# Optimization experiments

Measured on AMD Instinct MI355X. Metric: run time of the kernel, lower is better.

## Reference

```python
import jax, jax.numpy as jnp
import numpy as np

N_NODES = 245760      # 8192 graphs * 30 atoms
N_GRAPHS = 8192
N_EDGES = 1000000
NODES_PER_GRAPH = 30
F_NODE = 78
F_CELL = 1000
HID = 64


def _lin(key, fan_in, fan_out):
    kw, kb = jax.random.split(key)
    s = 1.0 / np.sqrt(fan_in)
    W = jax.random.uniform(kw, (fan_in, fan_out), minval=-s, maxval=s, dtype=jnp.float32)
    b = jax.random.uniform(kb, (fan_out,), minval=-s, maxval=s, dtype=jnp.float32)
    return W, b


def setup_inputs() -> dict:
    key = jax.random.key(0)
    ks = jax.random.split(key, 14)
    x = jax.random.normal(ks[0], (N_NODES, F_NODE), dtype=jnp.float32)
    # edges constrained within each graph: node = graph_id * 30 + local offset
    offs = jax.random.randint(ks[1], (2, N_EDGES), 0, NODES_PER_GRAPH)
    ge = jax.random.randint(ks[2], (N_EDGES,), 0, N_GRAPHS)
    edge_index = (ge[None, :] * NODES_PER_GRAPH + offs).astype(jnp.int64)
    batch = jnp.repeat(jnp.arange(N_GRAPHS, dtype=jnp.int64), NODES_PER_GRAPH)
    cell_features = jax.random.normal(ks[3], (N_GRAPHS, F_CELL), dtype=jnp.float32)
    W1, b1 = _lin(ks[4], F_NODE, HID)
    W2, b2 = _lin(ks[5], HID, 2 * HID)
    W3, b3 = _lin(ks[6], 2 * HID, 4 * HID)
    Wd, bd = _lin(ks[7], 4 * HID, HID)          # drug_embed_fc
    Wc1, bc1 = _lin(ks[8], F_CELL, 2 * HID)      # cell_fc1
    Wc2, bc2 = _lin(ks[9], 2 * HID, HID)         # cell_fc2
    Wm1, bm1 = _lin(ks[10], 2 * HID, HID)        # combiner_fc1
    Wm2, bm2 = _lin(ks[11], HID, 32)             # combiner_fc2
    Wo, bo = _lin(ks[12], 32, 1)                 # output_fc
    return {"x": x, "edge_index": edge_index, "batch": batch,
            "cell_features": cell_features,
            "W1": W1, "b1": b1, "W2": W2, "b2": b2, "W3": W3, "b3": b3,
            "Wd": Wd, "bd": bd, "Wc1": Wc1, "bc1": bc1, "Wc2": Wc2, "bc2": bc2,
            "Wm1": Wm1, "bm1": bm1, "Wm2": Wm2, "bm2": bm2, "Wo": Wo, "bo": bo}


def _gcn_conv(h, W, b, srcA, dstA, norm, n_nodes):
    # PyG GCNConv: linear transform, then sym-normalized scatter-add (self-loops included in srcA/dstA/norm)
    h = h @ W                                   # [N, out]
    msg = h[srcA] * norm[:, None]               # gather + edge scaling
    out = jnp.zeros((n_nodes, W.shape[1]), h.dtype).at[dstA].add(msg)
    return out + b


def reference(x, edge_index, batch, cell_features,
              W1, b1, W2, b2, W3, b3, Wd, bd,
              Wc1, bc1, Wc2, bc2, Wm1, bm1, Wm2, bm2, Wo, bo):
    n = x.shape[0]
    loops = jnp.arange(n, dtype=edge_index.dtype)
    srcA = jnp.concatenate([edge_index[0], loops])
    dstA = jnp.concatenate([edge_index[1], loops])
    deg = jax.ops.segment_sum(jnp.ones_like(dstA, dtype=x.dtype), dstA, num_segments=n)
    dinv = jax.lax.rsqrt(deg)                   # deg >= 1 due to self-loops
    norm = dinv[srcA] * dinv[dstA]

    h = jax.nn.relu(_gcn_conv(x, W1, b1, srcA, dstA, norm, n))
    h = jax.nn.relu(_gcn_conv(h, W2, b2, srcA, dstA, norm, n))
    h = jax.nn.relu(_gcn_conv(h, W3, b3, srcA, dstA, norm, n))

    # global mean pool over graphs
    sums = jax.ops.segment_sum(h, batch, num_segments=N_GRAPHS)
    cnts = jax.ops.segment_sum(jnp.ones((n,), h.dtype), batch, num_segments=N_GRAPHS)
    drug = (sums / cnts[:, None]) @ Wd + bd     # [B, HID]

    cell = jax.nn.relu(cell_features @ Wc1 + bc1)
    cell = cell @ Wc2 + bc2                      # [B, HID]

    comb = jnp.concatenate([drug, cell], axis=1)
    z = jax.nn.relu(comb @ Wm1 + bm1)
    z = jax.nn.relu(z @ Wm2 + bm2)
    out = z @ Wo + bo
    return out.reshape(-1)
```

## Files before the change

kernel.cpp:

```cpp
#include <hip/hip_runtime.h>

typedef __attribute__((ext_vector_type(8))) short short8;
typedef __attribute__((ext_vector_type(4))) short short4v;
typedef __attribute__((ext_vector_type(4))) float f32x4;
typedef unsigned short u16;

__device__ __forceinline__ u16 f2bf(float f) {
    union { float f; unsigned u; } v; v.f = f;
    unsigned r = v.u + 0x7FFFu + ((v.u >> 16) & 1u);
    return (u16)(r >> 16);
}
__device__ __forceinline__ float bf2f(u16 h) {
    union { unsigned u; float f; } v; v.u = ((unsigned)h) << 16;
    return v.f;
}
__device__ __forceinline__ void split2(float f, u16& h, u16& l) {
    h = f2bf(f);
    l = f2bf(f - bf2f(h));
}
__device__ __forceinline__ short8 ld8(const u16* p) {
    short4v a = *(const short4v*)p;
    short4v b = *(const short4v*)(p + 4);
    short8 r;
    r[0] = a[0]; r[1] = a[1]; r[2] = a[2]; r[3] = a[3];
    r[4] = b[0]; r[5] = b[1]; r[6] = b[2]; r[7] = b[3];
    return r;
}
#define MFMA(A, B, C) __builtin_amdgcn_mfma_f32_16x16x32_bf16(A, B, C, 0, 0, 0)

__global__ __launch_bounds__(256) void k_prep(int4* __restrict__ A32z, int nz4,
        const float* __restrict__ W1, u16* __restrict__ W1h, u16* __restrict__ W1l,
        const float* __restrict__ W2, u16* __restrict__ W2h, u16* __restrict__ W2l,
        const float* __restrict__ W3, u16* __restrict__ W3h, u16* __restrict__ W3l,
        const float* __restrict__ Wc1, u16* __restrict__ Wc1h, u16* __restrict__ Wc1l,
        const float* __restrict__ Wd, u16* __restrict__ WdTh, u16* __restrict__ WdTl,
        const float* __restrict__ Wc2, u16* __restrict__ Wc2Th, u16* __restrict__ Wc2Tl,
        const float* __restrict__ Wm1, u16* __restrict__ Wm1Th, u16* __restrict__ Wm1Tl,
        const float* __restrict__ Wm2, u16* __restrict__ Wm2Th, u16* __restrict__ Wm2Tl) {
    int i = blockIdx.x * 256 + threadIdx.x;
    if (i < nz4) { A32z[i] = make_int4(0, 0, 0, 0); return; }
    i -= nz4;
    const float* W; u16 *th, *tl; int K, F, Kp;
    if (i < 6144)        { W = W1;  th = W1h;  tl = W1l;  K = 78;   F = 64;  Kp = 96; }
    else if (i < 14336)  { i -= 6144;   W = W2;  th = W2h;  tl = W2l;  K = 64;   F = 128; Kp = 64; }
    else if (i < 47104)  { i -= 14336;  W = W3;  th = W3h;  tl = W3l;  K = 128;  F = 256; Kp = 128; }
    else if (i < 178176) { i -= 47104;  W = Wc1; th = Wc1h; tl = Wc1l; K = 1000; F = 128; Kp = 1024; }
    else if (i < 194560) { i -= 178176; W = Wd;  th = WdTh; tl = WdTl; K = 256;  F = 64;  Kp = 256; }
    else if (i < 202752) { i -= 194560; W = Wc2; th = Wc2Th; tl = Wc2Tl; K = 128; F = 64; Kp = 128; }
    else if (i < 210944) { i -= 202752; W = Wm1; th = Wm1Th; tl = Wm1Tl; K = 128; F = 64; Kp = 128; }
    else if (i < 212992) { i -= 210944; W = Wm2; th = Wm2Th; tl = Wm2Tl; K = 64;  F = 32; Kp = 64; }
    else return;
    int f = i / Kp, k = i - f * Kp;
    float v = (k < K) ? W[(size_t)k * F + f] : 0.f;
    u16 h, l; split2(v, h, l);
    th[i] = h; tl[i] = l;
}

__global__ void k_cnt(const int* __restrict__ ei, unsigned* __restrict__ A32, int E) {
    int e = blockIdx.x * 256 + threadIdx.x;
    if (e >= E) return;
    int s = ei[e], d = ei[E + e];
    int g = d / 30;
    int idx = g * 960 + (d - g * 30) * 32 + (s - g * 30);
    atomicAdd(&A32[idx >> 1], 1u << ((idx & 1) * 16));
}

__global__ __launch_bounds__(512, 8) void k_nodecell(
    const float* __restrict__ x, const unsigned* __restrict__ A32,
    const u16* __restrict__ W1h, const u16* __restrict__ W1l,
    const u16* __restrict__ W2h, const u16* __restrict__ W2l,
    const u16* __restrict__ W3h, const u16* __restrict__ W3l,
    const float* __restrict__ b1, const float* __restrict__ b2,
    const float* __restrict__ b3, float* __restrict__ P,
    const float* __restrict__ cf,
    const u16* __restrict__ Wc1h, const u16* __restrict__ Wc1l,
    const float* __restrict__ bc1, float* __restrict__ cell1,
    int CELLB) {
    __shared__ __align__(16) char smem[39936];
    int t = threadIdx.x;
    int wave = t >> 6, lane = t & 63, quad = lane >> 4, l15 = lane & 15;

    if (blockIdx.x < CELLB) {
        u16* Xh = (u16*)(smem + 0);
        u16* Xl = (u16*)(smem + 17920);
        int row0 = blockIdx.x * 64;
        int half = wave >> 2, wq = wave & 3;
        f32x4 acc[2][2] = {{{0.f,0.f,0.f,0.f},{0.f,0.f,0.f,0.f}},
                           {{0.f,0.f,0.f,0.f},{0.f,0.f,0.f,0.f}}};
        for (int ko = 0; ko < 8; ko++) {
#pragma unroll
            for (int ii = 0; ii < 4; ii++) {
                int i = t + ii * 512;
                int r = i >> 5, c4 = i & 31;
                int col = ko * 128 + c4 * 4;
                float4 v = {0.f, 0.f, 0.f, 0.f};
                if (col < 1000) v = *(const float4*)(cf + (size_t)(row0 + r) * 1000 + col);
                float vv[4] = {v.x, v.y, v.z, v.w};
                short4v hs, ls;
#pragma unroll
                for (int j = 0; j < 4; j++) {
                    u16 h, l; split2(vv[j], h, l);
                    hs[j] = (short)h; ls[j] = (short)l;
                }
                *(short4v*)(Xh + r * 140 + c4 * 4) = hs;
                *(short4v*)(Xl + r * 140 + c4 * 4) = ls;
            }
            __syncthreads();
#pragma unroll
            for (int kk = 0; kk < 4; kk++) {
                int klo = kk * 32 + quad * 8;
                short8 ah[2], al[2];
#pragma unroll
                for (int mi = 0; mi < 2; mi++) {
                    ah[mi] = ld8(&Xh[(half * 32 + mi * 16 + l15) * 140 + klo]);
                    al[mi] = ld8(&Xl[(half * 32 + mi * 16 + l15) * 140 + klo]);
                }
#pragma unroll
                for (int ni = 0; ni < 2; ni++) {
                    int col = wq * 32 + ni * 16 + l15;
                    size_t o = (size_t)col * 1024 + ko * 128 + kk * 32 + quad * 8;
                    short8 bh = *(const short8*)(Wc1h + o);
                    short8 bl = *(const short8*)(Wc1l + o);
#pragma unroll
                    for (int mi = 0; mi < 2; mi++) {
                        acc[mi][ni] = MFMA(ah[mi], bh, acc[mi][ni]);
                        acc[mi][ni] = MFMA(al[mi], bh, acc[mi][ni]);
                        acc[mi][ni] = MFMA(ah[mi], bl, acc[mi][ni]);
                    }
                }
            }
            __syncthreads();
        }
#pragma unroll
        for (int ni = 0; ni < 2; ni++) {
            int col = wq * 32 + ni * 16 + l15;
            float bv = bc1[col];
#pragma unroll
            for (int mi = 0; mi < 2; mi++)
#pragma unroll
                for (int rg = 0; rg < 4; rg++) {
                    int row = row0 + half * 32 + mi * 16 + quad * 4 + rg;
                    cell1[(size_t)row * 128 + col] = fmaxf(acc[mi][ni][rg] + bv, 0.f);
                }
        }
        return;
    }

    int g = blockIdx.x - CELLB;
    u16* xh  = (u16*)(smem + 0);
    u16* xl  = (u16*)(smem + 6400);
    u16* h1h = (u16*)(smem + 0);
    u16* h1l = (u16*)(smem + 4352);
    u16* a3h = (u16*)(smem + 0);
    u16* a3l = (u16*)(smem + 8448);
    float* Afp = (float*)(smem + 16896);
    float* dv  = (float*)(smem + 20736);
    u16* t1h = (u16*)(smem + 16896);
    u16* t1l = (u16*)(smem + 21504);
    u16* h2h = (u16*)(smem + 16896);
    u16* h2l = (u16*)(smem + 26112);
    u16* Ah  = (u16*)(smem + 35328);
    u16* Al  = (u16*)(smem + 37632);

    {
        for (int i = t; i < 860; i += 512) {
            uint* arr = (uint*)((i >= 430) ? (char*)xl : (char*)xh);
            int j = (i >= 430) ? i - 430 : i;
            int r, c32;
            if (j < 330) { r = j / 11; c32 = 39 + j % 11; }
            else { r = 30 + (j - 330) / 50; c32 = (j - 330) % 50; }
            arr[r * 50 + c32] = 0;
        }
        const float4* xg = (const float4*)(x + (size_t)g * 2340);
        for (int i = t; i < 585; i += 512) {
            float4 v = xg[i];
            int base = i * 4;
            float vv[4] = {v.x, v.y, v.z, v.w};
#pragma unroll
            for (int j = 0; j < 4; j++) {
                int idx = base + j;
                int r = idx / 78, c = idx - r * 78;
                u16 h, l; split2(vv[j], h, l);
                xh[r * 100 + c] = h; xl[r * 100 + c] = l;
            }
        }
        const unsigned* ac = A32 + (size_t)g * 480;
        for (int i = t; i < 480; i += 512) {
            unsigned w = ac[i];
            Afp[2 * i] = (float)(w & 0xFFFFu);
            Afp[2 * i + 1] = (float)(w >> 16);
        }
        if (t < 32) {
            float s = 1.f;
            if (t < 30) {
                const unsigned* rp = ac + t * 16;
                unsigned acc = 0;
#pragma unroll
                for (int j = 0; j < 16; j++) { unsigned w = rp[j]; acc += (w & 0xFFFFu) + (w >> 16); }
                s += (float)acc;
            }
            dv[t] = (t < 30) ? rsqrtf(s) : 0.f;
        }
    }
    __syncthreads();
    {
#pragma unroll
        for (int ii = 0; ii < 2; ii++) {
            int i = t + ii * 512;
            int r = i >> 5, c = i & 31;
            float a = 0.f;
            if (r < 30 && c < 30)
                a = (Afp[r * 32 + c] + (r == c ? 1.f : 0.f)) * dv[r] * dv[c];
            u16 h, l; split2(a, h, l);
            Ah[r * 36 + c] = h; Al[r * 36 + c] = l;
        }
    }
    __syncthreads();
    {
        int wm = wave >> 2, wn = wave & 3;
        int arow = wm * 16 + l15;
        int col = wn * 16 + l15;
        const u16* wph = W1h + col * 96 + quad * 8;
        const u16* wpl = W1l + col * 96 + quad * 8;
        f32x4 acc = {0.f, 0.f, 0.f, 0.f};
#pragma unroll
        for (int ch = 0; ch < 3; ch++) {
            int kc = ch * 32;
            short8 bh = *(const short8*)(wph + kc);
            short8 bl = *(const short8*)(wpl + kc);
            short8 ah = ld8(&xh[arow * 100 + kc + quad * 8]);
            short8 al = ld8(&xl[arow * 100 + kc + quad * 8]);
            acc = MFMA(ah, bh, acc);
            acc = MFMA(al, bh, acc);
            acc = MFMA(ah, bl, acc);
        }
#pragma unroll
        for (int rg = 0; rg < 4; rg++) {
            int row = wm * 16 + quad * 4 + rg;
            u16 h, l; split2(acc[rg], h, l);
            t1h[col * 36 + row] = h;
            t1l[col * 36 + row] = l;
        }
    }
    __syncthreads();
    {
        int wm = wave >> 2, wn = wave & 3;
        int arow = wm * 16 + l15;
        int col = wn * 16 + l15;
        short8 aAh = ld8(&Ah[arow * 36 + quad * 8]);
        short8 aAl = ld8(&Al[arow * 36 + quad * 8]);
        short8 bh = ld8(&t1h[col * 36 + quad * 8]);
        short8 bl = ld8(&t1l[col * 36 + quad * 8]);
        f32x4 acc = {0.f, 0.f, 0.f, 0.f};
        acc = MFMA(aAh, bh, acc);
        acc = MFMA(aAl, bh, acc);
        acc = MFMA(aAh, bl, acc);
        float bb = b1[col];
#pragma unroll
        for (int rg = 0; rg < 4; rg++) {
            int row = wm * 16 + quad * 4 + rg;
            float v = fmaxf(acc[rg] + bb, 0.f);
            u16 h, l; split2(v, h, l);
            h1h[row * 68 + col] = h;
            h1l[row * 68 + col] = l;
        }
    }
    __syncthreads();
    {
        int col = wave * 16 + l15;
        const u16* wph = W2h + col * 64 + quad * 8;
        const u16* wpl = W2l + col * 64 + quad * 8;
        f32x4 acc[2] = {{0.f,0.f,0.f,0.f},{0.f,0.f,0.f,0.f}};
#pragma unroll
        for (int ch = 0; ch < 2; ch++) {
            int kc = ch * 32;
            short8 bh = *(const short8*)(wph + kc);
            short8 bl = *(const short8*)(wpl + kc);
#pragma unroll
            for (int mi = 0; mi < 2; mi++) {
                short8 ah = ld8(&h1h[(mi * 16 + l15) * 68 + kc + quad * 8]);
                short8 al = ld8(&h1l[(mi * 16 + l15) * 68 + kc + quad * 8]);
                acc[mi] = MFMA(ah, bh, acc[mi]);
                acc[mi] = MFMA(al, bh, acc[mi]);
                acc[mi] = MFMA(ah, bl, acc[mi]);
            }
        }
        float bb = b2[col];
#pragma unroll
        for (int mi = 0; mi < 2; mi++)
#pragma unroll
            for (int rg = 0; rg < 4; rg++) {
                int row = mi * 16 + quad * 4 + rg;
                float v = fmaxf(acc[mi][rg] + bb, 0.f);
                u16 h, l; split2(v, h, l);
                h2h[col * 36 + row] = h;
                h2l[col * 36 + row] = l;
            }
    }
    __syncthreads();
    {
        int col = wave * 16 + l15;
        short8 bh = ld8(&h2h[col * 36 + quad * 8]);
        short8 bl = ld8(&h2l[col * 36 + quad * 8]);
        f32x4 acc[2] = {{0.f,0.f,0.f,0.f},{0.f,0.f,0.f,0.f}};
#pragma unroll
        for (int mi = 0; mi < 2; mi++) {
            short8 aAh = ld8(&Ah[(mi * 16 + l15) * 36 + quad * 8]);
            short8 aAl = ld8(&Al[(mi * 16 + l15) * 36 + quad * 8]);
            acc[mi] = MFMA(aAh, bh, acc[mi]);
            acc[mi] = MFMA(aAl, bh, acc[mi]);
            acc[mi] = MFMA(aAh, bl, acc[mi]);
        }
#pragma unroll
        for (int mi = 0; mi < 2; mi++)
#pragma unroll
            for (int rg = 0; rg < 4; rg++) {
                int row = mi * 16 + quad * 4 + rg;
                u16 h, l; split2(acc[mi][rg], h, l);
                a3h[row * 132 + col] = h;
                a3l[row * 132 + col] = l;
            }
    }
    __syncthreads();
    {
        int colb = wave * 32;
        f32x4 acc[2][2] = {{{0.f,0.f,0.f,0.f},{0.f,0.f,0.f,0.f}},
                           {{0.f,0.f,0.f,0.f},{0.f,0.f,0.f,0.f}}};
        short8 cwh[2], cwl[2], nwh[2], nwl[2];
#pragma unroll
        for (int ni = 0; ni < 2; ni++) {
            size_t o = (size_t)(colb + ni * 16 + l15) * 128 + quad * 8;
            cwh[ni] = *(const short8*)(W3h + o);
            cwl[ni] = *(const short8*)(W3l + o);
        }
#pragma unroll
        for (int ch = 0; ch < 4; ch++) {
            if (ch < 3) {
#pragma unroll
                for (int ni = 0; ni < 2; ni++) {
                    size_t o = (size_t)(colb + ni * 16 + l15) * 128 + (ch + 1) * 32 + quad * 8;
                    nwh[ni] = *(const short8*)(W3h + o);
                    nwl[ni] = *(const short8*)(W3l + o);
                }
            }
            short8 ah[2], al[2];
#pragma unroll
            for (int mi = 0; mi < 2; mi++) {
                ah[mi] = ld8(&a3h[(mi * 16 + l15) * 132 + ch * 32 + quad * 8]);
                al[mi] = ld8(&a3l[(mi * 16 + l15) * 132 + ch * 32 + quad * 8]);
            }
#pragma unroll
            for (int mi = 0; mi < 2; mi++)
#pragma unroll
                for (int ni = 0; ni < 2; ni++) {
                    acc[mi][ni] = MFMA(ah[mi], cwh[ni], acc[mi][ni]);
                    acc[mi][ni] = MFMA(al[mi], cwh[ni], acc[mi][ni]);
                    acc[mi][ni] = MFMA(ah[mi], cwl[ni], acc[mi][ni]);
                }
            if (ch < 3) {
#pragma unroll
                for (int ni = 0; ni < 2; ni++) { cwh[ni] = nwh[ni]; cwl[ni] = nwl[ni]; }
            }
        }
#pragma unroll
        for (int ni = 0; ni < 2; ni++) {
            int col = colb + ni * 16 + l15;
            float bb = b3[col];
            float p = 0.f;
#pragma unroll
            for (int mi = 0; mi < 2; mi++)
#pragma unroll
                for (int rg = 0; rg < 4; rg++) {
                    int row = mi * 16 + quad * 4 + rg;
                    if (row < 30) p += fmaxf(acc[mi][ni][rg] + bb, 0.f);
                }
            p += __shfl_down(p, 32);
            p += __shfl_down(p, 16);
            if (lane < 16)
                P[(size_t)g * 256 + colb + ni * 16 + lane] = p * (1.0f / 30.0f);
        }
    }
}

__global__ __launch_bounds__(256) void k_tail2(const float* __restrict__ pooled,
        const float* __restrict__ cell1,
        const u16* __restrict__ WdTh, const u16* __restrict__ WdTl, const float* __restrict__ bd,
        const u16* __restrict__ Wc2Th, const u16* __restrict__ Wc2Tl, const float* __restrict__ bc2,
        const u16* __restrict__ Wm1Th, const u16* __restrict__ Wm1Tl, const float* __restrict__ bm1,
        const u16* __restrict__ Wm2Th, const u16* __restrict__ Wm2Tl, const float* __restrict__ bm2,
        const float* __restrict__ Wo, const float* __restrict__ bo,
        float* __restrict__ out) {
    __shared__ __align__(16) char smem[50176];
    u16* Xh  = (u16*)(smem);
    u16* Xl  = (u16*)(smem + 25088);
    u16* dzh = (u16*)(smem);
    u16* dzl = (u16*)(smem + 8960);
    u16* z1h = (u16*)(smem + 17920);
    u16* z1l = (u16*)(smem + 22528);
    float* z2f = (float*)(smem + 27136);
    int t = threadIdx.x;
    int row0 = blockIdx.x * 32;
    int wave = t >> 6, lane = t & 63, quad = lane >> 4, l15 = lane & 15;

#pragma unroll
    for (int ii = 0; ii < 12; ii++) {
        int i = t + ii * 256;
        int r = i / 96, c4 = i - r * 96;
        float4 v = (c4 < 64)
            ? ((const float4*)(pooled + (size_t)(row0 + r) * 256))[c4]
            : ((const float4*)(cell1 + (size_t)(row0 + r) * 128))[c4 - 64];
        float vv[4] = {v.x, v.y, v.z, v.w};
        short4v hs, ls;
#pragma unroll
        for (int j = 0; j < 4; j++) {
            u16 h, l; split2(vv[j], h, l);
            hs[j] = (short)h; ls[j] = (short)l;
        }
        *(short4v*)(Xh + r * 392 + c4 * 4) = hs;
        *(short4v*)(Xl + r * 392 + c4 * 4) = ls;
    }
    __syncthreads();

    bool cw = wave >= 2;
    int nbase = (wave & 1) * 32;
    const u16* Bh = cw ? Wc2Th : WdTh;
    const u16* Bl = cw ? Wc2Tl : WdTl;
    const int Kp = cw ? 128 : 256;
    const int nch = cw ? 4 : 8;
    const int acol = cw ? 256 : 0;
    f32x4 acc[2][2] = {{{0.f,0.f,0.f,0.f},{0.f,0.f,0.f,0.f}},
                       {{0.f,0.f,0.f,0.f},{0.f,0.f,0.f,0.f}}};
    for (int ch = 0; ch < nch; ch++) {
        int kc = ch * 32 + quad * 8;
        short8 ah[2], al[2];
#pragma unroll
        for (int mi = 0; mi < 2; mi++) {
            ah[mi] = ld8(&Xh[(mi * 16 + l15) * 392 + acol + kc]);
            al[mi] = ld8(&Xl[(mi * 16 + l15) * 392 + acol + kc]);
        }
#pragma unroll
        for (int ni = 0; ni < 2; ni++) {
            int col = nbase + ni * 16 + l15;
            short8 bh = *(const short8*)(Bh + (size_t)col * Kp + kc);
            short8 bl = *(const short8*)(Bl + (size_t)col * Kp + kc);
#pragma unroll
            for (int mi = 0; mi < 2; mi++) {
                acc[mi][ni] = MFMA(ah[mi], bh, acc[mi][ni]);
                acc[mi][ni] = MFMA(al[mi], bh, acc[mi][ni]);
                acc[mi][ni] = MFMA(ah[mi], bl, acc[mi][ni]);
            }
        }
    }
    __syncthreads();
#pragma unroll
    for (int ni = 0; ni < 2; ni++) {
        int c = nbase + ni * 16 + l15;
        float bb = cw ? bc2[c] : bd[c];
        int col = (cw ? 64 : 0) + c;
#pragma unroll
        for (int mi = 0; mi < 2; mi++)
#pragma unroll
            for (int rg = 0; rg < 4; rg++) {
                int row = mi * 16 + quad * 4 + rg;
                u16 h, l; split2(acc[mi][ni][rg] + bb, h, l);
                dzh[row * 140 + col] = h;
                dzl[row * 140 + col] = l;
            }
    }
    __syncthreads();

    {
        int col = wave * 16 + l15;
        f32x4 a2[2] = {{0.f,0.f,0.f,0.f},{0.f,0.f,0.f,0.f}};
#pragma unroll
        for (int ch = 0; ch < 4; ch++) {
            int kc = ch * 32 + quad * 8;
            short8 bh = *(const short8*)(Wm1Th + (size_t)col * 128 + kc);
            short8 bl = *(const short8*)(Wm1Tl + (size_t)col * 128 + kc);
#pragma unroll
            for (int mi = 0; mi < 2; mi++) {
                short8 ah = ld8(&dzh[(mi * 16 + l15) * 140 + kc]);
                short8 al = ld8(&dzl[(mi * 16 + l15) * 140 + kc]);
                a2[mi] = MFMA(ah, bh, a2[mi]);
                a2[mi] = MFMA(al, bh, a2[mi]);
                a2[mi] = MFMA(ah, bl, a2[mi]);
            }
        }
        float bb = bm1[col];
#pragma unroll
        for (int mi = 0; mi < 2; mi++)
#pragma unroll
            for (int rg = 0; rg < 4; rg++) {
                int row = mi * 16 + quad * 4 + rg;
                u16 h, l; split2(fmaxf(a2[mi][rg] + bb, 0.f), h, l);
                z1h[row * 72 + col] = h;
                z1l[row * 72 + col] = l;
            }
    }
    __syncthreads();

    if (wave < 2) {
        int col = wave * 16 + l15;
        f32x4 a3[2] = {{0.f,0.f,0.f,0.f},{0.f,0.f,0.f,0.f}};
#pragma unroll
        for (int ch = 0; ch < 2; ch++) {
            int kc = ch * 32 + quad * 8;
            short8 bh = *(const short8*)(Wm2Th + (size_t)col * 64 + kc);
            short8 bl = *(const short8*)(Wm2Tl + (size_t)col * 64 + kc);
#pragma unroll
            for (int mi = 0; mi < 2; mi++) {
                short8 ah = ld8(&z1h[(mi * 16 + l15) * 72 + kc]);
                short8 al = ld8(&z1l[(mi * 16 + l15) * 72 + kc]);
                a3[mi] = MFMA(ah, bh, a3[mi]);
                a3[mi] = MFMA(al, bh, a3[mi]);
                a3[mi] = MFMA(ah, bl, a3[mi]);
            }
        }
        float bb = bm2[col];
#pragma unroll
        for (int mi = 0; mi < 2; mi++)
#pragma unroll
            for (int rg = 0; rg < 4; rg++) {
                int row = mi * 16 + quad * 4 + rg;
                z2f[row * 33 + col] = fmaxf(a3[mi][rg] + bb, 0.f);
            }
    }
    __syncthreads();

    if (t < 32) {
        float s = bo[0];
#pragma unroll 8
        for (int k = 0; k < 32; k++) s += z2f[t * 33 + k] * Wo[k];
        out[row0 + t] = s;
    }
}


extern "C" void kernel_launch(void* const* d_in, const int* in_sizes, int n_in,
                              void* d_out, int out_size, void* d_ws, size_t ws_size,
                              hipStream_t stream) {
    const float* x   = (const float*)d_in[0];
    const int*   ei  = (const int*)d_in[1];
    const float* cf  = (const float*)d_in[3];
    const float* W1  = (const float*)d_in[4];
    const float* b1  = (const float*)d_in[5];
    const float* W2  = (const float*)d_in[6];
    const float* b2  = (const float*)d_in[7];
    const float* W3  = (const float*)d_in[8];
    const float* b3  = (const float*)d_in[9];
    const float* Wd  = (const float*)d_in[10];
    const float* bd  = (const float*)d_in[11];
    const float* Wc1 = (const float*)d_in[12];
    const float* bc1 = (const float*)d_in[13];
    const float* Wc2 = (const float*)d_in[14];
    const float* bc2 = (const float*)d_in[15];
    const float* Wm1 = (const float*)d_in[16];
    const float* bm1 = (const float*)d_in[17];
    const float* Wm2 = (const float*)d_in[18];
    const float* bm2 = (const float*)d_in[19];
    const float* Wo  = (const float*)d_in[20];
    const float* bo  = (const float*)d_in[21];
    float* out = (float*)d_out;

    const int E = in_sizes[1] / 2;
    const int B = in_sizes[3] / 1000;

    char* w = (char*)d_ws;
    auto carve = [&](size_t bytes) { void* p = (void*)w; w += (bytes + 255) & ~(size_t)255; return p; };
    unsigned* A32 = (unsigned*)carve((size_t)B * 960 * 2);
    float* pooled = (float*)carve((size_t)B * 256 * 4);
    float* cell1  = (float*)carve((size_t)B * 128 * 4);
    u16* W1th = (u16*)carve(64 * 96 * 2);     u16* W1tl = (u16*)carve(64 * 96 * 2);
    u16* W2th = (u16*)carve(128 * 64 * 2);    u16* W2tl = (u16*)carve(128 * 64 * 2);
    u16* W3th = (u16*)carve(256 * 128 * 2);   u16* W3tl = (u16*)carve(256 * 128 * 2);
    u16* Wc1th = (u16*)carve(128 * 1024 * 2); u16* Wc1tl = (u16*)carve(128 * 1024 * 2);
    u16* WdTh = (u16*)carve(64 * 256 * 2);    u16* WdTl = (u16*)carve(64 * 256 * 2);
    u16* Wc2Th = (u16*)carve(64 * 128 * 2);   u16* Wc2Tl = (u16*)carve(64 * 128 * 2);
    u16* Wm1Th = (u16*)carve(64 * 128 * 2);   u16* Wm1Tl = (u16*)carve(64 * 128 * 2);
    u16* Wm2Th = (u16*)carve(32 * 64 * 2);    u16* Wm2Tl = (u16*)carve(32 * 64 * 2);

    auto g1 = [](int n) { return (n + 255) / 256; };

    const int nz4 = B * 120;
    const int nsplit = 212992;

    k_prep<<<g1(nz4 + nsplit), 256, 0, stream>>>((int4*)A32, nz4,
        W1, W1th, W1tl, W2, W2th, W2tl, W3, W3th, W3tl, Wc1, Wc1th, Wc1tl,
        Wd, WdTh, WdTl, Wc2, Wc2Th, Wc2Tl, Wm1, Wm1Th, Wm1Tl, Wm2, Wm2Th, Wm2Tl);

    k_cnt<<<g1(E), 256, 0, stream>>>(ei, A32, E);

    const int CELLB = B / 64;
    k_nodecell<<<CELLB + B, 512, 0, stream>>>(x, A32,
                                  W1th, W1tl, W2th, W2tl, W3th, W3tl,
                                  b1, b2, b3, pooled,
                                  cf, Wc1th, Wc1tl, bc1, cell1, CELLB);

    k_tail2<<<B / 32, 256, 0, stream>>>(pooled, cell1,
                                        WdTh, WdTl, bd, Wc2Th, Wc2Tl, bc2,
                                        Wm1Th, Wm1Tl, bm1, Wm2Th, Wm2Tl, bm2,
                                        Wo, bo, out);
}
```

Baseline: 419.0 us.

## Move cell MLP into edge-count kernel and add MFMA priority hints

The cell_fc1 GEMM moves out of the node kernel into a new mixed kernel. That kernel also does the edge-count atomics and the splitting of the small weights, so the atomic-bound counting overlaps with the compute-bound cell GEMM. A tiny pre-kernel now only zeroes the adjacency buffer and splits Wc1. s_setprio hints are placed around the MFMA groups to favour waves issuing matrix work. Kernel launches stay at four, and the node kernel now runs only graph blocks.

```diff
diff --git a/kernel.cpp b/kernel.cpp
--- a/kernel.cpp
+++ b/kernel.cpp
@@ -27,63 +27,42 @@
     return r;
 }
 #define MFMA(A, B, C) __builtin_amdgcn_mfma_f32_16x16x32_bf16(A, B, C, 0, 0, 0)
-
-__global__ __launch_bounds__(256) void k_prep(int4* __restrict__ A32z, int nz4,
+#define PRIO1() __builtin_amdgcn_s_setprio(1)
+#define PRIO0() __builtin_amdgcn_s_setprio(0)
+
+__global__ __launch_bounds__(256) void k_pre(int4* __restrict__ A32z, int nz4,
+        const float* __restrict__ Wc1, u16* __restrict__ Wc1h, u16* __restrict__ Wc1l) {
+    int i = blockIdx.x * 256 + threadIdx.x;
+    if (i < nz4) { A32z[i] = make_int4(0, 0, 0, 0); return; }
+    i -= nz4;
+    if (i >= 131072) return;
+    int f = i >> 10, k = i & 1023;
+    float v = (k < 1000) ? Wc1[(size_t)k * 128 + f] : 0.f;
+    u16 h, l; split2(v, h, l);
+    Wc1h[i] = h; Wc1l[i] = l;
+}
+
+__global__ __launch_bounds__(512, 8) void k_mix(
+        const int* __restrict__ ei, unsigned* __restrict__ A32, int E, int NCNT,
+        const float* __restrict__ cf,
+        const u16* __restrict__ Wc1h, const u16* __restrict__ Wc1l,
+        const float* __restrict__ bc1, float* __restrict__ cell1, int CELLB,
         const float* __restrict__ W1, u16* __restrict__ W1h, u16* __restrict__ W1l,
         const float* __restrict__ W2, u16* __restrict__ W2h, u16* __restrict__ W2l,
         const float* __restrict__ W3, u16* __restrict__ W3h, u16* __restrict__ W3l,
-        const float* __restrict__ Wc1, u16* __restrict__ Wc1h, u16* __restrict__ Wc1l,
         const float* __restrict__ Wd, u16* __restrict__ WdTh, u16* __restrict__ WdTl,
         const float* __restrict__ Wc2, u16* __restrict__ Wc2Th, u16* __restrict__ Wc2Tl,
         const float* __restrict__ Wm1, u16* __restrict__ Wm1Th, u16* __restrict__ Wm1Tl,
         const float* __restrict__ Wm2, u16* __restrict__ Wm2Th, u16* __restrict__ Wm2Tl) {
-    int i = blockIdx.x * 256 + threadIdx.x;
-    if (i < nz4) { A32z[i] = make_int4(0, 0, 0, 0); return; }
-    i -= nz4;
-    const float* W; u16 *th, *tl; int K, F, Kp;
-    if (i < 6144)        { W = W1;  th = W1h;  tl = W1l;  K = 78;   F = 64;  Kp = 96; }
-    else if (i < 14336)  { i -= 6144;   W = W2;  th = W2h;  tl = W2l;  K = 64;   F = 128; Kp = 64; }
-    else if (i < 47104)  { i -= 14336;  W = W3;  th = W3h;  tl = W3l;  K = 128;  F = 256; Kp = 128; }
-    else if (i < 178176) { i -= 47104;  W = Wc1; th = Wc1h; tl = Wc1l; K = 1000; F = 128; Kp = 1024; }
-    else if (i < 194560) { i -= 178176; W = Wd;  th = WdTh; tl = WdTl; K = 256;  F = 64;  Kp = 256; }
-    else if (i < 202752) { i -= 194560; W = Wc2; th = Wc2Th; tl = Wc2Tl; K = 128; F = 64; Kp = 128; }
-    else if (i < 210944) { i -= 202752; W = Wm1; th = Wm1Th; tl = Wm1Tl; K = 128; F = 64; Kp = 128; }
-    else if (i < 212992) { i -= 210944; W = Wm2; th = Wm2Th; tl = Wm2Tl; K = 64;  F = 32; Kp = 64; }
-    else return;
-    int f = i / Kp, k = i - f * Kp;
-    float v = (k < K) ? W[(size_t)k * F + f] : 0.f;
-    u16 h, l; split2(v, h, l);
-    th[i] = h; tl[i] = l;
-}
-
-__global__ void k_cnt(const int* __restrict__ ei, unsigned* __restrict__ A32, int E) {
-    int e = blockIdx.x * 256 + threadIdx.x;
-    if (e >= E) return;
-    int s = ei[e], d = ei[E + e];
-    int g = d / 30;
-    int idx = g * 960 + (d - g * 30) * 32 + (s - g * 30);
-    atomicAdd(&A32[idx >> 1], 1u << ((idx & 1) * 16));
-}
-
-__global__ __launch_bounds__(512, 8) void k_nodecell(
-    const float* __restrict__ x, const unsigned* __restrict__ A32,
-    const u16* __restrict__ W1h, const u16* __restrict__ W1l,
-    const u16* __restrict__ W2h, const u16* __restrict__ W2l,
-    const u16* __restrict__ W3h, const u16* __restrict__ W3l,
-    const float* __restrict__ b1, const float* __restrict__ b2,
-    const float* __restrict__ b3, float* __restrict__ P,
-    const float* __restrict__ cf,
-    const u16* __restrict__ Wc1h, const u16* __restrict__ Wc1l,
-    const float* __restrict__ bc1, float* __restrict__ cell1,
-    int CELLB) {
-    __shared__ __align__(16) char smem[39936];
+    __shared__ __align__(16) char smem[35840];
     int t = threadIdx.x;
-    int wave = t >> 6, lane = t & 63, quad = lane >> 4, l15 = lane & 15;
-
-    if (blockIdx.x < CELLB) {
+    int bb = blockIdx.x;
+
+    if (bb < CELLB) {
         u16* Xh = (u16*)(smem + 0);
         u16* Xl = (u16*)(smem + 17920);
-        int row0 = blockIdx.x * 64;
+        int row0 = bb * 64;
+        int wave = t >> 6, lane = t & 63, quad = lane >> 4, l15 = lane & 15;
         int half = wave >> 2, wq = wave & 3;
         f32x4 acc[2][2] = {{{0.f,0.f,0.f,0.f},{0.f,0.f,0.f,0.f}},
                            {{0.f,0.f,0.f,0.f},{0.f,0.f,0.f,0.f}}};
@@ -121,12 +100,14 @@
                     size_t o = (size_t)col * 1024 + ko * 128 + kk * 32 + quad * 8;
                     short8 bh = *(const short8*)(Wc1h + o);
                     short8 bl = *(const short8*)(Wc1l + o);
+                    PRIO1();
 #pragma unroll
                     for (int mi = 0; mi < 2; mi++) {
                         acc[mi][ni] = MFMA(ah[mi], bh, acc[mi][ni]);
                         acc[mi][ni] = MFMA(al[mi], bh, acc[mi][ni]);
                         acc[mi][ni] = MFMA(ah[mi], bl, acc[mi][ni]);
                     }
+                    PRIO0();
                 }
             }
             __syncthreads();
@@ -145,8 +126,48 @@
         }
         return;
     }
-
-    int g = blockIdx.x - CELLB;
+    bb -= CELLB;
+
+    if (bb < NCNT) {
+        int e = bb * 512 + t;
+        if (e < E) {
+            int s = ei[e], d = ei[E + e];
+            int g = d / 30;
+            int idx = g * 960 + (d - g * 30) * 32 + (s - g * 30);
+            atomicAdd(&A32[idx >> 1], 1u << ((idx & 1) * 16));
+        }
+        return;
+    }
+    bb -= NCNT;
+
+    int i = bb * 512 + t;
+    const float* W; u16 *th, *tl; int K, F, Kp;
+    if (i < 6144)        { W = W1;  th = W1h;  tl = W1l;  K = 78;   F = 64;  Kp = 96; }
+    else if (i < 14336)  { i -= 6144;   W = W2;  th = W2h;  tl = W2l;  K = 64;   F = 128; Kp = 64; }
+    else if (i < 47104)  { i -= 14336;  W = W3;  th = W3h;  tl = W3l;  K = 128;  F = 256; Kp = 128; }
+    else if (i < 63488)  { i -= 47104;  W = Wd;  th = WdTh; tl = WdTl; K = 256;  F = 64;  Kp = 256; }
+    else if (i < 71680)  { i -= 63488;  W = Wc2; th = Wc2Th; tl = Wc2Tl; K = 128; F = 64; Kp = 128; }
+    else if (i < 79872)  { i -= 71680;  W = Wm1; th = Wm1Th; tl = Wm1Tl; K = 128; F = 64; Kp = 128; }
+    else if (i < 81920)  { i -= 79872;  W = Wm2; th = Wm2Th; tl = Wm2Tl; K = 64;  F = 32; Kp = 64; }
+    else return;
+    int f = i / Kp, k = i - f * Kp;
+    float v = (k < K) ? W[(size_t)k * F + f] : 0.f;
+    u16 h, l; split2(v, h, l);
+    th[i] = h; tl[i] = l;
+}
+
+__global__ __launch_bounds__(512, 8) void k_node(
+    const float* __restrict__ x, const unsigned* __restrict__ A32,
+    const u16* __restrict__ W1h, const u16* __restrict__ W1l,
+    const u16* __restrict__ W2h, const u16* __restrict__ W2l,
+    const u16* __restrict__ W3h, const u16* __restrict__ W3l,
+    const float* __restrict__ b1, const float* __restrict__ b2,
+    const float* __restrict__ b3, float* __restrict__ P) {
+    __shared__ __align__(16) char smem[39936];
+    int t = threadIdx.x;
+    int g = blockIdx.x;
+    int wave = t >> 6, lane = t & 63, quad = lane >> 4, l15 = lane & 15;
+
     u16* xh  = (u16*)(smem + 0);
     u16* xl  = (u16*)(smem + 6400);
     u16* h1h = (u16*)(smem + 0);
@@ -230,9 +251,11 @@
             short8 bl = *(const short8*)(wpl + kc);
             short8 ah = ld8(&xh[arow * 100 + kc + quad * 8]);
             short8 al = ld8(&xl[arow * 100 + kc + quad * 8]);
+            PRIO1();
             acc = MFMA(ah, bh, acc);
             acc = MFMA(al, bh, acc);
             acc = MFMA(ah, bl, acc);
+            PRIO0();
         }
 #pragma unroll
         for (int rg = 0; rg < 4; rg++) {
@@ -252,9 +275,11 @@
         short8 bh = ld8(&t1h[col * 36 + quad * 8]);
         short8 bl = ld8(&t1l[col * 36 + quad * 8]);
         f32x4 acc = {0.f, 0.f, 0.f, 0.f};
+        PRIO1();
         acc = MFMA(aAh, bh, acc);
         acc = MFMA(aAl, bh, acc);
         acc = MFMA(aAh, bl, acc);
+        PRIO0();
         float bb = b1[col];
 #pragma unroll
         for (int rg = 0; rg < 4; rg++) {
@@ -280,9 +305,11 @@
             for (int mi = 0; mi < 2; mi++) {
                 short8 ah = ld8(&h1h[(mi * 16 + l15) * 68 + kc + quad * 8]);
                 short8 al = ld8(&h1l[(mi * 16 + l15) * 68 + kc + quad * 8]);
+                PRIO1();
                 acc[mi] = MFMA(ah, bh, acc[mi]);
                 acc[mi] = MFMA(al, bh, acc[mi]);
                 acc[mi] = MFMA(ah, bl, acc[mi]);
+                PRIO0();
             }
         }
         float bb = b2[col];
@@ -307,9 +334,11 @@
         for (int mi = 0; mi < 2; mi++) {
             short8 aAh = ld8(&Ah[(mi * 16 + l15) * 36 + quad * 8]);
             short8 aAl = ld8(&Al[(mi * 16 + l15) * 36 + quad * 8]);
+            PRIO1();
             acc[mi] = MFMA(aAh, bh, acc[mi]);
             acc[mi] = MFMA(aAl, bh, acc[mi]);
             acc[mi] = MFMA(aAh, bl, acc[mi]);
+            PRIO0();
         }
 #pragma unroll
         for (int mi = 0; mi < 2; mi++)
@@ -349,6 +378,7 @@
                 ah[mi] = ld8(&a3h[(mi * 16 + l15) * 132 + ch * 32 + quad * 8]);
                 al[mi] = ld8(&a3l[(mi * 16 + l15) * 132 + ch * 32 + quad * 8]);
             }
+            PRIO1();
 #pragma unroll
             for (int mi = 0; mi < 2; mi++)
 #pragma unroll
@@ -357,6 +387,7 @@
                     acc[mi][ni] = MFMA(al[mi], cwh[ni], acc[mi][ni]);
                     acc[mi][ni] = MFMA(ah[mi], cwl[ni], acc[mi][ni]);
                 }
+            PRIO0();
             if (ch < 3) {
 #pragma unroll
                 for (int ni = 0; ni < 2; ni++) { cwh[ni] = nwh[ni]; cwl[ni] = nwl[ni]; }
@@ -579,22 +610,22 @@
     u16* Wm1Th = (u16*)carve(64 * 128 * 2);   u16* Wm1Tl = (u16*)carve(64 * 128 * 2);
     u16* Wm2Th = (u16*)carve(32 * 64 * 2);    u16* Wm2Tl = (u16*)carve(32 * 64 * 2);
 
-    auto g1 = [](int n) { return (n + 255) / 256; };
-
     const int nz4 = B * 120;
-    const int nsplit = 212992;
-
-    k_prep<<<g1(nz4 + nsplit), 256, 0, stream>>>((int4*)A32, nz4,
-        W1, W1th, W1tl, W2, W2th, W2tl, W3, W3th, W3tl, Wc1, Wc1th, Wc1tl,
+
+    k_pre<<<(nz4 + 131072 + 255) / 256, 256, 0, stream>>>((int4*)A32, nz4, Wc1, Wc1th, Wc1tl);
+
+    const int CELLB = B / 64;
+    const int NCNT = (E + 511) / 512;
+    const int NSPL = (81920 + 511) / 512;
+    k_mix<<<CELLB + NCNT + NSPL, 512, 0, stream>>>(
+        ei, A32, E, NCNT,
+        cf, Wc1th, Wc1tl, bc1, cell1, CELLB,
+        W1, W1th, W1tl, W2, W2th, W2tl, W3, W3th, W3tl,
         Wd, WdTh, WdTl, Wc2, Wc2Th, Wc2Tl, Wm1, Wm1Th, Wm1Tl, Wm2, Wm2Th, Wm2Tl);
 
-    k_cnt<<<g1(E), 256, 0, stream>>>(ei, A32, E);
-
-    const int CELLB = B / 64;
-    k_nodecell<<<CELLB + B, 512, 0, stream>>>(x, A32,
+    k_node<<<B, 512, 0, stream>>>(x, A32,
                                   W1th, W1tl, W2th, W2tl, W3th, W3tl,
-                                  b1, b2, b3, pooled,
-                                  cf, Wc1th, Wc1tl, bc1, cell1, CELLB);
+                                  b1, b2, b3, pooled);
 
     k_tail2<<<B / 32, 256, 0, stream>>>(pooled, cell1,
                                         WdTh, WdTl, bd, Wc2Th, Wc2Tl, bc2,
```

New measurement: 502.0 us. 19.8% more time.
